# Kernel optimization log

Measured on AMD Instinct MI355X. Metric: run time of the kernel, lower is better.

## Reference

```python
import math
import jax, jax.numpy as jnp
import numpy as np


def setup_inputs() -> dict:
    key = jax.random.key(0)
    k1, k2, k3 = jax.random.split(key, 3)
    n, c, h, w = 4, 128, 64, 64
    return {
        "key": jax.random.normal(k1, (n, c, h, w), dtype=jnp.float32),
        "query": jax.random.normal(k2, (n, c, h, w), dtype=jnp.float32),
        "value": jax.random.normal(k3, (n, c, h, w), dtype=jnp.float32),
    }


def reference(key, query, value):
    n, c, h, w = key.shape
    c2 = value.shape[1]
    hw = h * w
    k = key.reshape(n, c, hw)      # (n, c, hw)
    q = query.reshape(n, c, hw)    # (n, c, hw)
    v = value.reshape(n, c2, hw)   # (n, c2, hw)
    # scores[n, s, t] = sum_c k[n,c,s] * q[n,c,t], scaled by sqrt(c)
    scores = jnp.einsum("ncs,nct->nst", k, q) / math.sqrt(c)
    # softmax over dim=-2 (the key-token axis s)
    p_attn = jax.nn.softmax(scores, axis=-2)
    # p_val[n, e, t] = sum_s v[n,e,s] * p_attn[n,s,t]
    p_val = jnp.einsum("nes,nst->net", v, p_attn)
    return p_val.reshape(n, c2, h, w)
```

## Files before the change

kernel.cpp:

```cpp
#include <hip/hip_runtime.h>


#define HW 4096
#define CC 128

typedef _Float16 half8  __attribute__((ext_vector_type(8)));
typedef _Float16 half4v __attribute__((ext_vector_type(4)));
typedef float    float4v __attribute__((ext_vector_type(4)));

#define KSCALE 0.12751743f
#define CEXP   8.656170245f

__device__ __forceinline__ float fast_exp2(float x) {
  return __builtin_amdgcn_exp2f(x);
}

__device__ __forceinline__ void async_copy16(void* lds, const void* g) {
  __builtin_amdgcn_global_load_lds(
      (const __attribute__((address_space(1))) unsigned int*)g,
      (__attribute__((address_space(3))) unsigned int*)lds, 16, 0, 0);
}

__global__ __launch_bounds__(256)
void prepass(const float* __restrict__ K, const float* __restrict__ Q,
             const float* __restrict__ V, _Float16* __restrict__ KT,
             _Float16* __restrict__ QT, _Float16* __restrict__ Vh) {
  const int bid = blockIdx.x;
  const int tid = threadIdx.x;
  if (bid < 2048) {
    __shared__ float tile[32][65];
    const bool isK = bid < 1024;
    const int id = bid & 1023;
    const float* in = isK ? K : Q;
    _Float16* out = isK ? KT : QT;
    const float scale = isK ? KSCALE : 1.0f;
    const int c0 = (id & 3) << 5;
    const int s0 = ((id >> 2) & 63) << 6;
    const int b  = id >> 8;
    const float* ib = in + (size_t)b * CC * HW;
    _Float16* ob = out + (size_t)b * HW * CC;
    const int r  = tid >> 4;
    const int c4 = (tid & 15) * 4;
    *(float4*)&tile[r][c4]      = *(const float4*)(ib + (size_t)(c0 + r) * HW + s0 + c4);
    *(float4*)&tile[r + 16][c4] = *(const float4*)(ib + (size_t)(c0 + r + 16) * HW + s0 + c4);
    __syncthreads();
    const int s  = tid >> 2;
    const int c8 = (tid & 3) * 8;
    half8 h;
    #pragma unroll
    for (int k = 0; k < 8; ++k) h[k] = (_Float16)(tile[c8 + k][s] * scale);
    *(half8*)&ob[(size_t)(s0 + s) * CC + c0 + c8] = h;
  } else {
    const int id = bid - 2048;
    #pragma unroll
    for (int p = 0; p < 4; ++p) {
      const int f = id * 1024 + p * 256 + tid;
      const float4v v = *(const float4v*)(V + 4 * (size_t)f);
      half4v h;
      h.x = (_Float16)v.x; h.y = (_Float16)v.y; h.z = (_Float16)v.z; h.w = (_Float16)v.w;
      *(half4v*)(Vh + 4 * (size_t)f) = h;
    }
  }
}

__global__ __launch_bounds__(512, 4)
void attn_mfma(const _Float16* __restrict__ KT, const _Float16* __restrict__ QT,
               const _Float16* __restrict__ Vh, float* __restrict__ Og) {
  __shared__ __align__(16) _Float16 sK[2][64][128];
  __shared__ __align__(16) _Float16 sV[2][128][64];
  __shared__ __align__(16) _Float16 sPT[8][16][40];
  __shared__ float sLred[4][2][16];

  const int tid  = threadIdx.x;
  const int b    = blockIdx.x >> 6;
  const int tt0  = (blockIdx.x & 63) << 6;
  const int w    = tid >> 6;
  const int lane = tid & 63;
  const int q    = lane >> 4;
  const int tc   = lane & 15;
  const int g    = w >> 1;
  const int sl   = w & 1;

  const _Float16* KTb = KT + (size_t)b * HW * CC;
  const _Float16* Vb  = Vh + (size_t)b * CC * HW;
  float* Ob = Og + (size_t)b * CC * HW;

  half8 qf[4];
  {
    const _Float16* qp = QT + (size_t)b * HW * CC + (size_t)(tt0 + 16 * g + tc) * CC + 8 * q;
    #pragma unroll
    for (int ks = 0; ks < 4; ++ks) qf[ks] = *(const half8*)(qp + 32 * ks);
  }

  const int krow_l = lane >> 4, kchn = lane & 15;
  const int vrow_l = lane >> 3, vchn = lane & 7;
  #define STAGE(sn, buf)                                                        \
    {                                                                           \
      _Pragma("unroll")                                                         \
      for (int p = 0; p < 2; ++p) {                                             \
        const int kr = w * 8 + p * 4 + krow_l;                                  \
        const int kg = kchn ^ (kr & 15);                                        \
        async_copy16(&sK[buf][w * 8 + p * 4][0],                                \
                     KTb + (size_t)((sn) + kr) * CC + kg * 8);                  \
        const int vr = w * 16 + p * 8 + vrow_l;                                 \
        const int vg = vchn ^ (vr & 7);                                         \
        async_copy16(&sV[buf][w * 16 + p * 8][0],                               \
                     Vb + (size_t)vr * HW + (sn) + vg * 8);                     \
      }                                                                         \
    }

  STAGE(0, 0);

  float4v accO[8];
  #pragma unroll
  for (int i2 = 0; i2 < 8; ++i2) accO[i2] = (float4v){0.f, 0.f, 0.f, 0.f};
  float l_part = 0.0f;

  __syncthreads();

  for (int it = 0; it < HW / 64; ++it) {
    const int buf = it & 1;
    if (it + 1 < HW / 64) STAGE((it + 1) * 64, buf ^ 1);

    float4v acc[2];
    acc[0] = (float4v){0.f, 0.f, 0.f, 0.f};
    acc[1] = (float4v){0.f, 0.f, 0.f, 0.f};
    #pragma unroll
    for (int ks = 0; ks < 4; ++ks) {
      #pragma unroll
      for (int j = 0; j < 2; ++j) {
        const int row = 32 * sl + 16 * j + tc;
        const half8 a = *(const half8*)&sK[buf][row][((4 * ks + q) ^ tc) * 8];
        acc[j] = __builtin_amdgcn_mfma_f32_16x16x32_f16(a, qf[ks], acc[j], 0, 0, 0);
      }
    }

    #pragma unroll
    for (int j = 0; j < 2; ++j) {
      const float p0 = fast_exp2(acc[j].x - CEXP);
      const float p1 = fast_exp2(acc[j].y - CEXP);
      const float p2 = fast_exp2(acc[j].z - CEXP);
      const float p3 = fast_exp2(acc[j].w - CEXP);
      l_part += (p0 + p1) + (p2 + p3);
      half4v h;
      h.x = (_Float16)p0; h.y = (_Float16)p1; h.z = (_Float16)p2; h.w = (_Float16)p3;
      *(half4v*)&sPT[w][tc][16 * j + 4 * q] = h;
    }

    const half8 bp = *(const half8*)&sPT[w][tc][8 * q];
    #pragma unroll
    for (int i2 = 0; i2 < 8; ++i2) {
      const half8 av = *(const half8*)&sV[buf][16 * i2 + tc][(((4 * sl + q) ^ (tc & 7))) * 8];
      accO[i2] = __builtin_amdgcn_mfma_f32_16x16x32_f16(av, bp, accO[i2], 0, 0, 0);
    }

    __syncthreads();
  }

  l_part += __shfl_xor(l_part, 16);
  l_part += __shfl_xor(l_part, 32);
  if (lane < 16) sLred[g][sl][tc] = l_part;

  float* mbuf = (float*)&sK[0][0][0];
  if (sl == 1) {
    #pragma unroll
    for (int i2 = 0; i2 < 8; ++i2)
      *(float4v*)&mbuf[g * 2048 + tc * 128 + 16 * i2 + 4 * q] = accO[i2];
  }
  __syncthreads();
  if (sl == 0) {
    const float li = 1.0f / (sLred[g][0][tc] + sLred[g][1][tc]);
    const int t = tt0 + 16 * g + tc;
    #pragma unroll
    for (int i2 = 0; i2 < 8; ++i2) {
      const float4v o = *(const float4v*)&mbuf[g * 2048 + tc * 128 + 16 * i2 + 4 * q];
      const int e0 = 16 * i2 + 4 * q;
      Ob[(size_t)(e0 + 0) * HW + t] = (accO[i2].x + o.x) * li;
      Ob[(size_t)(e0 + 1) * HW + t] = (accO[i2].y + o.y) * li;
      Ob[(size_t)(e0 + 2) * HW + t] = (accO[i2].z + o.z) * li;
      Ob[(size_t)(e0 + 3) * HW + t] = (accO[i2].w + o.w) * li;
    }
  }
}

extern "C" void kernel_launch(void* const* d_in, const int* in_sizes, int n_in,
                              void* d_out, int out_size, void* d_ws, size_t ws_size,
                              hipStream_t stream) {
  const float* key   = (const float*)d_in[0];
  const float* query = (const float*)d_in[1];
  const float* value = (const float*)d_in[2];
  float* out = (float*)d_out;

  const size_t TEN = (size_t)4 * HW * CC * sizeof(_Float16);
  _Float16* KT = (_Float16*)d_ws;
  _Float16* QT = (_Float16*)((char*)d_ws + TEN);
  _Float16* Vh = (_Float16*)((char*)d_ws + 2 * TEN);
  (void)ws_size;

  prepass<<<dim3(2560), dim3(256), 0, stream>>>(key, query, value, KT, QT, Vh);
  attn_mfma<<<dim3(256), dim3(512), 0, stream>>>(KT, QT, Vh, out);
}
```

Baseline: 150.6 us.

## Split attention over key axis into two halves with merge kernel

Adds a split-K attention kernel where each block handles half the key tokens. This doubles the grid to 512 blocks so more of the GPU's CUs get work. A merge kernel then sums the partial outputs and normalizers. A fallback 1024-thread kernel with a 128-token stage runs when the workspace is too small. The split path adds a 16MB partial-output write and read plus an extra launch.

Measured after the change: 129.6 us. 13.9% less time.

```diff
diff --git a/kernel.cpp b/kernel.cpp
--- a/kernel.cpp
+++ b/kernel.cpp
@@ -3,13 +3,13 @@
 
 #define HW 4096
 #define CC 128
+#define KSCALE 0.12751743f
+#define CEXP   8.656170245f
+#define SMEMB  152576
 
 typedef _Float16 half8  __attribute__((ext_vector_type(8)));
 typedef _Float16 half4v __attribute__((ext_vector_type(4)));
 typedef float    float4v __attribute__((ext_vector_type(4)));
-
-#define KSCALE 0.12751743f
-#define CEXP   8.656170245f
 
 __device__ __forceinline__ float fast_exp2(float x) {
   return __builtin_amdgcn_exp2f(x);
@@ -64,16 +64,20 @@
 }
 
 __global__ __launch_bounds__(512, 4)
-void attn_mfma(const _Float16* __restrict__ KT, const _Float16* __restrict__ QT,
-               const _Float16* __restrict__ Vh, float* __restrict__ Og) {
+void attn_split(const _Float16* __restrict__ KT, const _Float16* __restrict__ QT,
+                const _Float16* __restrict__ Vh, float* __restrict__ Opart,
+                float* __restrict__ lpart) {
   __shared__ __align__(16) _Float16 sK[2][64][128];
   __shared__ __align__(16) _Float16 sV[2][128][64];
   __shared__ __align__(16) _Float16 sPT[8][16][40];
   __shared__ float sLred[4][2][16];
 
+  const int bid  = blockIdx.x;
+  const int half = bid >> 8;
+  const int b    = (bid >> 6) & 3;
+  const int tt0  = (bid & 63) << 6;
+  const int soff = half << 11;
   const int tid  = threadIdx.x;
-  const int b    = blockIdx.x >> 6;
-  const int tt0  = (blockIdx.x & 63) << 6;
   const int w    = tid >> 6;
   const int lane = tid & 63;
   const int q    = lane >> 4;
@@ -83,7 +87,7 @@
 
   const _Float16* KTb = KT + (size_t)b * HW * CC;
   const _Float16* Vb  = Vh + (size_t)b * CC * HW;
-  float* Ob = Og + (size_t)b * CC * HW;
+  float* Op = Opart + (size_t)(half * 4 + b) * CC * HW;
 
   half8 qf[4];
   {
@@ -94,22 +98,22 @@
 
   const int krow_l = lane >> 4, kchn = lane & 15;
   const int vrow_l = lane >> 3, vchn = lane & 7;
-  #define STAGE(sn, buf)                                                        \
+  #define STAGE_S(sn, buf)                                                      \
     {                                                                           \
       _Pragma("unroll")                                                         \
       for (int p = 0; p < 2; ++p) {                                             \
         const int kr = w * 8 + p * 4 + krow_l;                                  \
         const int kg = kchn ^ (kr & 15);                                        \
         async_copy16(&sK[buf][w * 8 + p * 4][0],                                \
-                     KTb + (size_t)((sn) + kr) * CC + kg * 8);                  \
+                     KTb + (size_t)(soff + (sn) + kr) * CC + kg * 8);           \
         const int vr = w * 16 + p * 8 + vrow_l;                                 \
         const int vg = vchn ^ (vr & 7);                                         \
         async_copy16(&sV[buf][w * 16 + p * 8][0],                               \
-                     Vb + (size_t)vr * HW + (sn) + vg * 8);                     \
+                     Vb + (size_t)vr * HW + soff + (sn) + vg * 8);              \
       }                                                                         \
     }
 
-  STAGE(0, 0);
+  STAGE_S(0, 0);
 
   float4v accO[8];
   #pragma unroll
@@ -118,9 +122,9 @@
 
   __syncthreads();
 
-  for (int it = 0; it < HW / 64; ++it) {
+  for (int it = 0; it < 2048 / 64; ++it) {
     const int buf = it & 1;
-    if (it + 1 < HW / 64) STAGE((it + 1) * 64, buf ^ 1);
+    if (it + 1 < 2048 / 64) STAGE_S((it + 1) * 64, buf ^ 1);
 
     float4v acc[2];
     acc[0] = (float4v){0.f, 0.f, 0.f, 0.f};
@@ -169,16 +173,169 @@
   }
   __syncthreads();
   if (sl == 0) {
-    const float li = 1.0f / (sLred[g][0][tc] + sLred[g][1][tc]);
     const int t = tt0 + 16 * g + tc;
+    if (lane < 16) lpart[(size_t)(half * 4 + b) * HW + t] = sLred[g][0][tc] + sLred[g][1][tc];
     #pragma unroll
     for (int i2 = 0; i2 < 8; ++i2) {
       const float4v o = *(const float4v*)&mbuf[g * 2048 + tc * 128 + 16 * i2 + 4 * q];
       const int e0 = 16 * i2 + 4 * q;
-      Ob[(size_t)(e0 + 0) * HW + t] = (accO[i2].x + o.x) * li;
-      Ob[(size_t)(e0 + 1) * HW + t] = (accO[i2].y + o.y) * li;
-      Ob[(size_t)(e0 + 2) * HW + t] = (accO[i2].z + o.z) * li;
-      Ob[(size_t)(e0 + 3) * HW + t] = (accO[i2].w + o.w) * li;
+      Op[(size_t)(e0 + 0) * HW + t] = accO[i2].x + o.x;
+      Op[(size_t)(e0 + 1) * HW + t] = accO[i2].y + o.y;
+      Op[(size_t)(e0 + 2) * HW + t] = accO[i2].z + o.z;
+      Op[(size_t)(e0 + 3) * HW + t] = accO[i2].w + o.w;
+    }
+  }
+}
+
+__global__ __launch_bounds__(256)
+void merge_split(const float* __restrict__ Op, const float* __restrict__ lp,
+                 float* __restrict__ out) {
+  const int f   = blockIdx.x * 256 + threadIdx.x;
+  const int row = f >> 10;
+  const int t4  = (f & 1023) << 2;
+  const int b   = row >> 7;
+  const float4v oa = *(const float4v*)(Op + (size_t)row * HW + t4);
+  const float4v ob = *(const float4v*)(Op + ((size_t)row + 512) * HW + t4);
+  const float4v la = *(const float4v*)(lp + (size_t)b * HW + t4);
+  const float4v lb = *(const float4v*)(lp + ((size_t)b + 4) * HW + t4);
+  float4v o;
+  o.x = (oa.x + ob.x) / (la.x + lb.x);
+  o.y = (oa.y + ob.y) / (la.y + lb.y);
+  o.z = (oa.z + ob.z) / (la.z + lb.z);
+  o.w = (oa.w + ob.w) / (la.w + lb.w);
+  *(float4v*)(out + (size_t)row * HW + t4) = o;
+}
+
+__device__ __forceinline__ _Float16* pK(char* s, int buf, int row) {
+  return (_Float16*)s + ((size_t)buf * 128 + row) * 128;
+}
+__device__ __forceinline__ _Float16* pV(char* s, int buf, int row) {
+  return (_Float16*)(s + 65536) + ((size_t)buf * 128 + row) * 128;
+}
+__device__ __forceinline__ _Float16* pP(char* s, int w, int t) {
+  return (_Float16*)(s + 131072) + ((size_t)w * 16 + t) * 40;
+}
+__device__ __forceinline__ float* pL(char* s, int g, int sl) {
+  return (float*)(s + 151552) + ((size_t)g * 4 + sl) * 16;
+}
+
+__global__ __launch_bounds__(1024, 4)
+void attn_mfma(const _Float16* __restrict__ KT, const _Float16* __restrict__ QT,
+               const _Float16* __restrict__ Vh, float* __restrict__ Og) {
+  __shared__ __align__(16) char smem[SMEMB];
+  const int bid = blockIdx.x, tid = threadIdx.x;
+  const int b    = bid >> 6;
+  const int tt0  = (bid & 63) << 6;
+  const int w    = tid >> 6;
+  const int lane = tid & 63;
+  const int q    = lane >> 4;
+  const int tc   = lane & 15;
+  const int g    = w >> 2;
+  const int sl   = w & 3;
+
+  const _Float16* KTb = KT + (size_t)b * HW * CC;
+  const _Float16* Vb  = Vh + (size_t)b * CC * HW;
+  float* Ob = Og + (size_t)b * CC * HW;
+
+  half8 qf[4];
+  {
+    const _Float16* qp = QT + (size_t)b * HW * CC + (size_t)(tt0 + 16 * g + tc) * CC + 8 * q;
+    #pragma unroll
+    for (int ks = 0; ks < 4; ++ks) qf[ks] = *(const half8*)(qp + 32 * ks);
+  }
+
+  const int r0    = w * 8;
+  const int lrow  = lane >> 4;
+  const int lchnk = lane & 15;
+  auto STAGE = [&](int sn, int buf) {
+    #pragma unroll
+    for (int p = 0; p < 2; ++p) {
+      const int row = r0 + p * 4 + lrow;
+      const int gc  = lchnk ^ (row & 15);
+      async_copy16(pK(smem, buf, r0 + p * 4), KTb + (size_t)(sn + row) * CC + gc * 8);
+      async_copy16(pV(smem, buf, r0 + p * 4), Vb + (size_t)row * HW + sn + gc * 8);
+    }
+  };
+
+  STAGE(0, 0);
+
+  float4v accO[8];
+  #pragma unroll
+  for (int i2 = 0; i2 < 8; ++i2) accO[i2] = (float4v){0.f, 0.f, 0.f, 0.f};
+  float l_part = 0.0f;
+
+  __syncthreads();
+
+  for (int it = 0; it < HW / 128; ++it) {
+    const int buf = it & 1;
+    if (it + 1 < HW / 128) STAGE((it + 1) * 128, buf ^ 1);
+
+    float4v acc[2];
+    acc[0] = (float4v){0.f, 0.f, 0.f, 0.f};
+    acc[1] = (float4v){0.f, 0.f, 0.f, 0.f};
+    #pragma unroll
+    for (int ks = 0; ks < 4; ++ks) {
+      #pragma unroll
+      for (int j = 0; j < 2; ++j) {
+        const int row = 32 * sl + 16 * j + tc;
+        const half8 a = *(const half8*)(pK(smem, buf, row) + ((4 * ks + q) ^ tc) * 8);
+        acc[j] = __builtin_amdgcn_mfma_f32_16x16x32_f16(a, qf[ks], acc[j], 0, 0, 0);
+      }
+    }
+
+    #pragma unroll
+    for (int j = 0; j < 2; ++j) {
+      const float p0 = fast_exp2(acc[j].x - CEXP);
+      const float p1 = fast_exp2(acc[j].y - CEXP);
+      const float p2 = fast_exp2(acc[j].z - CEXP);
+      const float p3 = fast_exp2(acc[j].w - CEXP);
+      l_part += (p0 + p1) + (p2 + p3);
+      half4v h;
+      h.x = (_Float16)p0; h.y = (_Float16)p1; h.z = (_Float16)p2; h.w = (_Float16)p3;
+      *(half4v*)(pP(smem, w, tc) + 16 * j + 4 * q) = h;
+    }
+
+    const half8 bp = *(const half8*)(pP(smem, w, tc) + 8 * q);
+    #pragma unroll
+    for (int i2 = 0; i2 < 8; ++i2) {
+      const half8 av = *(const half8*)(pV(smem, buf, 16 * i2 + tc) + ((4 * sl + q) ^ tc) * 8);
+      accO[i2] = __builtin_amdgcn_mfma_f32_16x16x32_f16(av, bp, accO[i2], 0, 0, 0);
+    }
+
+    __syncthreads();
+  }
+
+  l_part += __shfl_xor(l_part, 16);
+  l_part += __shfl_xor(l_part, 32);
+  if (lane < 16) pL(smem, g, sl)[tc] = l_part;
+
+  float* mbuf = (float*)smem;
+  if (sl != 0) {
+    #pragma unroll
+    for (int i2 = 0; i2 < 8; ++i2) {
+      const int c4s = (4 * i2 + q) ^ ((tc & 7) << 2);
+      *(float4v*)&mbuf[(size_t)(sl - 1) * 8192 + g * 2048 + tc * 128 + 4 * c4s] = accO[i2];
+    }
+  }
+  __syncthreads();
+  if (sl == 0) {
+    const float li = 1.0f / (((pL(smem, g, 0)[tc] + pL(smem, g, 1)[tc]) +
+                              (pL(smem, g, 2)[tc] + pL(smem, g, 3)[tc])));
+    const int t = tt0 + 16 * g + tc;
+    #pragma unroll
+    for (int i2 = 0; i2 < 8; ++i2) {
+      const int c4s = (4 * i2 + q) ^ ((tc & 7) << 2);
+      float4v o = accO[i2];
+      #pragma unroll
+      for (int r = 0; r < 3; ++r) {
+        const float4v m = *(const float4v*)&mbuf[(size_t)r * 8192 + g * 2048 + tc * 128 + 4 * c4s];
+        o.x += m.x; o.y += m.y; o.z += m.z; o.w += m.w;
+      }
+      const int e0 = 16 * i2 + 4 * q;
+      Ob[(size_t)(e0 + 0) * HW + t] = o.x * li;
+      Ob[(size_t)(e0 + 1) * HW + t] = o.y * li;
+      Ob[(size_t)(e0 + 2) * HW + t] = o.z * li;
+      Ob[(size_t)(e0 + 3) * HW + t] = o.w * li;
     }
   }
 }
@@ -191,12 +348,20 @@
   const float* value = (const float*)d_in[2];
   float* out = (float*)d_out;
 
-  const size_t TEN = (size_t)4 * HW * CC * sizeof(_Float16);
+  const size_t TEN   = (size_t)4 * HW * CC * sizeof(_Float16);
+  const size_t OPART = (size_t)2 * 4 * CC * HW * sizeof(float);
+  const size_t LPART = (size_t)2 * 4 * HW * sizeof(float);
   _Float16* KT = (_Float16*)d_ws;
   _Float16* QT = (_Float16*)((char*)d_ws + TEN);
   _Float16* Vh = (_Float16*)((char*)d_ws + 2 * TEN);
-  (void)ws_size;
+  float* Opart = (float*)((char*)d_ws + 3 * TEN);
+  float* lpart = (float*)((char*)d_ws + 3 * TEN + OPART);
 
   prepass<<<dim3(2560), dim3(256), 0, stream>>>(key, query, value, KT, QT, Vh);
-  attn_mfma<<<dim3(256), dim3(512), 0, stream>>>(KT, QT, Vh, out);
-}
+  if (ws_size >= 3 * TEN + OPART + LPART) {
+    attn_split<<<dim3(512), dim3(512), 0, stream>>>(KT, QT, Vh, Opart, lpart);
+    merge_split<<<dim3(2048), dim3(256), 0, stream>>>(Opart, lpart, out);
+  } else {
+    attn_mfma<<<dim3(256), dim3(1024), 0, stream>>>(KT, QT, Vh, out);
+  }
+}
```
